# Kernel tuning notes

Hardware: AMD Instinct MI355X
Metric: run time of the kernel (lower is better)

Reference implementation:

```python
import jax, jax.numpy as jnp
import numpy as np

N = 100_000   # nodes
E = 3_200_000 # edges (avg degree 32)
F = 256       # node feature dim
H = 5         # hidden_size (hard-coded in source)
C = 7         # num_classes (hard-coded in source)


def setup_inputs() -> dict:
    key = jax.random.key(0)
    ks = jax.random.split(key, 8)
    x = jax.random.normal(ks[0], (N, F), dtype=jnp.float32)
    edge_index = jax.random.randint(ks[1], (2, E), 0, N, dtype=jnp.int32)
    # GCNConv uses glorot init for weight, zeros for bias; Linear uses kaiming-ish.
    def glorot(k, fan_in, fan_out):
        s = jnp.sqrt(6.0 / (fan_in + fan_out))
        return jax.random.uniform(k, (fan_in, fan_out), jnp.float32, -s, s)
    W1 = glorot(ks[2], F, H)
    b1 = jnp.zeros((H,), jnp.float32)
    W2 = glorot(ks[3], H, H)
    b2 = jnp.zeros((H,), jnp.float32)
    s = 1.0 / jnp.sqrt(jnp.float32(H))
    W3 = jax.random.uniform(ks[4], (H, C), jnp.float32, -s, s)
    b3 = jax.random.uniform(ks[5], (C,), jnp.float32, -s, s)
    return {"x": x, "edge_index": edge_index,
            "W1": W1, "b1": b1, "W2": W2, "b2": b2, "W3": W3, "b3": b3}


def _gcn_conv(h_in, W, b, src, dst, deg_inv_sqrt, n):
    """PyG GCNConv: linear first, then D^-1/2 (A+I) D^-1/2 aggregation, then bias."""
    h = h_in @ W                                   # [N, out]
    norm = deg_inv_sqrt[src] * deg_inv_sqrt[dst]   # [E]
    agg = jax.ops.segment_sum(h[src] * norm[:, None], dst, num_segments=n)
    # self-loop contribution: weight = deg^-1 for each node
    agg = agg + h * (deg_inv_sqrt * deg_inv_sqrt)[:, None]
    return agg + b


def reference(x, edge_index, W1, b1, W2, b2, W3, b3):
    src, dst = edge_index[0], edge_index[1]
    n = x.shape[0]
    # degree with self-loops added (PyG add_self_loops + edge_weight=1)
    deg = jax.ops.segment_sum(jnp.ones_like(src, jnp.float32), dst, num_segments=n) + 1.0
    deg_inv_sqrt = jax.lax.rsqrt(deg)
    h = jax.nn.relu(_gcn_conv(x, W1, b1, src, dst, deg_inv_sqrt, n))
    h = jax.nn.relu(_gcn_conv(h, W2, b2, src, dst, deg_inv_sqrt, n))
    return h @ W3 + b3
```

## Files before the change

### kernel.cpp

```cpp
#include <hip/hip_runtime.h>

#define F_DIM 256
#define H 5
#define C 7
#define PAD 8

#define PART_SH 9
#define PART_NODES 512
#define PCAP 20480
#define TILE 2048
#define NPMAX 256
#define CSR_ROUNDS 20

__global__ __launch_bounds__(256) void k_xw1z(const float* __restrict__ x,
                                              const float* __restrict__ W1,
                                              float* __restrict__ hw1,
                                              int* __restrict__ gcur, int n) {
    if (blockIdx.x == 0 && threadIdx.x < NPMAX) gcur[threadIdx.x] = 0;
    int row = blockIdx.x * 256 + threadIdx.x;
    if (row >= n) return;
    const float4* xp = (const float4*)(x + (size_t)row * F_DIM);
    float acc[H] = {0.f, 0.f, 0.f, 0.f, 0.f};
#pragma unroll 8
    for (int f4 = 0; f4 < F_DIM / 4; ++f4) {
        float4 v = xp[f4];
        const float* wp = W1 + f4 * 4 * H;
#pragma unroll
        for (int c = 0; c < H; ++c)
            acc[c] += v.x * wp[c] + v.y * wp[H + c] + v.z * wp[2 * H + c] + v.w * wp[3 * H + c];
    }
    float* o = hw1 + (size_t)row * PAD;
    *reinterpret_cast<float4*>(o) = make_float4(acc[0], acc[1], acc[2], acc[3]);
    o[4] = acc[4];
}

__global__ __launch_bounds__(256) void k_part(const int* __restrict__ src,
                                              const int* __restrict__ dst,
                                              int* __restrict__ gcur,
                                              unsigned int* __restrict__ parr, int E) {
    __shared__ unsigned int s_out[TILE];
    __shared__ unsigned char s_op[TILE];
    __shared__ int s_wcur[4][NPMAX];
    __shared__ int s_hist[NPMAX];
    __shared__ int s_excl[NPMAX];
    __shared__ int s_gbase[NPMAX];

    const int t = threadIdx.x;
    const int w = t >> 6;
    const int t0 = blockIdx.x * TILE;

    for (int i = t; i < 4 * NPMAX; i += 256) ((int*)s_wcur)[i] = 0;
    __syncthreads();

    unsigned int pair[8];
    int pp[8], rk[8];
#pragma unroll
    for (int k = 0; k < 8; ++k) {
        int e = t0 + k * 256 + t;
        if (e < E) {
            int d = dst[e];
            int s = src[e];
            int p = d >> PART_SH;
            pair[k] = ((unsigned)s << PART_SH) | (unsigned)(d & (PART_NODES - 1));
            pp[k] = p;
            rk[k] = atomicAdd(&s_wcur[w][p], 1);
        } else {
            pp[k] = -1;
        }
    }
    __syncthreads();
    {
        int sum = 0;
#pragma unroll
        for (int ww = 0; ww < 4; ++ww) sum += s_wcur[ww][t];
        s_hist[t] = sum;
    }
    __syncthreads();
    if (t < 64) {
        int base = t * 4;
        int loc[4]; int tot = 0;
#pragma unroll
        for (int k = 0; k < 4; ++k) { loc[k] = tot; tot += s_hist[base + k]; }
        int incl = tot;
#pragma unroll
        for (int off = 1; off < 64; off <<= 1) {
            int u = __shfl_up(incl, off, 64);
            if (t >= off) incl += u;
        }
        int excl = incl - tot;
#pragma unroll
        for (int k = 0; k < 4; ++k) s_excl[base + k] = excl + loc[k];
    }
    __syncthreads();
    {
        int run = s_excl[t];
#pragma unroll
        for (int ww = 0; ww < 4; ++ww) { int c = s_wcur[ww][t]; s_wcur[ww][t] = run; run += c; }
        int cnt = s_hist[t];
        s_gbase[t] = (cnt > 0) ? atomicAdd(&gcur[t], cnt) : 0;
    }
    __syncthreads();
#pragma unroll
    for (int k = 0; k < 8; ++k) {
        if (pp[k] >= 0) {
            int pos = s_wcur[w][pp[k]] + rk[k];
            s_out[pos] = pair[k];
            s_op[pos] = (unsigned char)pp[k];
        }
    }
    __syncthreads();
    const int tilecnt = s_excl[NPMAX - 1] + s_hist[NPMAX - 1];
#pragma unroll
    for (int k = 0; k < 8; ++k) {
        int i = k * 256 + t;
        if (i < tilecnt) {
            int p = s_op[i];
            int gpos = s_gbase[p] + (i - s_excl[p]);
            if (gpos < PCAP)
                parr[(size_t)p * PCAP + gpos] = s_out[i];
        }
    }
}

__global__ __launch_bounds__(1024) void k_csr(
        const int* __restrict__ gcur, const unsigned int* __restrict__ parr,
        int* __restrict__ sorted, int2* __restrict__ rpd, float* __restrict__ dis,
        const float* __restrict__ hw1, float* __restrict__ hw1s, int n) {
    __shared__ int s_cnt[PART_NODES];
    __shared__ int s_excl[PART_NODES];
    const int p = blockIdx.x;
    const int t = threadIdx.x;
    int m = gcur[p]; if (m > PCAP) m = PCAP;
    const unsigned int* pp = parr + (size_t)p * PCAP;

    if (t < PART_NODES) s_cnt[t] = 0;
    __syncthreads();

    unsigned int pr[CSR_ROUNDS];
    int rk[CSR_ROUNDS];
#pragma unroll
    for (int k = 0; k < CSR_ROUNDS; ++k) {
        int i = k * 1024 + t;
        if (i < m) {
            pr[k] = pp[i];
            rk[k] = atomicAdd(&s_cnt[pr[k] & (PART_NODES - 1)], 1);
        }
    }
    __syncthreads();
    if (t < 64) {
        int base = t * 8;
        int loc[8]; int tot = 0;
#pragma unroll
        for (int k = 0; k < 8; ++k) { loc[k] = tot; tot += s_cnt[base + k]; }
        int incl = tot;
#pragma unroll
        for (int off = 1; off < 64; off <<= 1) {
            int u = __shfl_up(incl, off, 64);
            if (t >= off) incl += u;
        }
        int excl = incl - tot;
#pragma unroll
        for (int k = 0; k < 8; ++k) s_excl[base + k] = excl + loc[k];
    }
    __syncthreads();
    if (t < PART_NODES) {
        int node = p * PART_NODES + t;
        if (node < n) {
            int dg = s_cnt[t];
            rpd[node] = make_int2(p * PCAP + s_excl[t], dg);
            float di = rsqrtf((float)dg + 1.0f);
            dis[node] = di;
            const float* hp = hw1 + (size_t)node * PAD;
            float4 a = *(const float4*)hp;
            float h4 = hp[4];
            float* os = hw1s + (size_t)node * PAD;
            *reinterpret_cast<float4*>(os) = make_float4(a.x * di, a.y * di, a.z * di, a.w * di);
            os[4] = h4 * di;
        }
    }
#pragma unroll
    for (int k = 0; k < CSR_ROUNDS; ++k) {
        int i = k * 1024 + t;
        if (i < m) {
            int dloc = pr[k] & (PART_NODES - 1);
            sorted[(size_t)p * PCAP + s_excl[dloc] + rk[k]] = (int)(pr[k] >> PART_SH);
        }
    }
}

template<int OUTD, int OSTRIDE, bool ADD_B3, bool SCALE_OUT>
__global__ __launch_bounds__(256) void k_layer(
        const int* __restrict__ sorted, const int2* __restrict__ rpd,
        const float* __restrict__ dis,
        const float* __restrict__ hin, const float* __restrict__ bn,
        const float* __restrict__ Wnext, const float* __restrict__ b3,
        float* __restrict__ outp, int n) {
    int tid = blockIdx.x * blockDim.x + threadIdx.x;
    int node = tid >> 2, sub = tid & 3;
    if (node >= n) return;
    int2 rd = rpd[node];
    int deg = rd.y;
    const int* bp = sorted + rd.x;

    float acc[H] = {0.f, 0.f, 0.f, 0.f, 0.f};
    int j = sub;
    for (; j + 32 <= deg; j += 32) {
        int s0 = bp[j], s1 = bp[j + 4], s2 = bp[j + 8], s3 = bp[j + 12];
        int s4 = bp[j + 16], s5 = bp[j + 20], s6 = bp[j + 24], s7 = bp[j + 28];
        const float4* h0 = (const float4*)(hin + (size_t)s0 * PAD);
        const float4* h1 = (const float4*)(hin + (size_t)s1 * PAD);
        const float4* h2 = (const float4*)(hin + (size_t)s2 * PAD);
        const float4* h3 = (const float4*)(hin + (size_t)s3 * PAD);
        const float4* h4 = (const float4*)(hin + (size_t)s4 * PAD);
        const float4* h5 = (const float4*)(hin + (size_t)s5 * PAD);
        const float4* h6 = (const float4*)(hin + (size_t)s6 * PAD);
        const float4* h7 = (const float4*)(hin + (size_t)s7 * PAD);
        float4 a0 = h0[0], e0 = h0[1], a1 = h1[0], e1 = h1[1];
        float4 a2 = h2[0], e2 = h2[1], a3 = h3[0], e3 = h3[1];
        float4 a4 = h4[0], e4 = h4[1], a5 = h5[0], e5 = h5[1];
        float4 a6 = h6[0], e6 = h6[1], a7 = h7[0], e7 = h7[1];
        acc[0] += (a0.x + a1.x + a2.x + a3.x) + (a4.x + a5.x + a6.x + a7.x);
        acc[1] += (a0.y + a1.y + a2.y + a3.y) + (a4.y + a5.y + a6.y + a7.y);
        acc[2] += (a0.z + a1.z + a2.z + a3.z) + (a4.z + a5.z + a6.z + a7.z);
        acc[3] += (a0.w + a1.w + a2.w + a3.w) + (a4.w + a5.w + a6.w + a7.w);
        acc[4] += (e0.x + e1.x + e2.x + e3.x) + (e4.x + e5.x + e6.x + e7.x);
    }
    for (; j + 16 <= deg; j += 16) {
        int s0 = bp[j], s1 = bp[j + 4], s2 = bp[j + 8], s3 = bp[j + 12];
        const float4* h0 = (const float4*)(hin + (size_t)s0 * PAD);
        const float4* h1 = (const float4*)(hin + (size_t)s1 * PAD);
        const float4* h2 = (const float4*)(hin + (size_t)s2 * PAD);
        const float4* h3 = (const float4*)(hin + (size_t)s3 * PAD);
        float4 a0 = h0[0], e0 = h0[1], a1 = h1[0], e1 = h1[1];
        float4 a2 = h2[0], e2 = h2[1], a3 = h3[0], e3 = h3[1];
        acc[0] += a0.x + a1.x + a2.x + a3.x;
        acc[1] += a0.y + a1.y + a2.y + a3.y;
        acc[2] += a0.z + a1.z + a2.z + a3.z;
        acc[3] += a0.w + a1.w + a2.w + a3.w;
        acc[4] += e0.x + e1.x + e2.x + e3.x;
    }
    for (; j + 8 <= deg; j += 8) {
        int s0 = bp[j], s1 = bp[j + 4];
        const float4* h0 = (const float4*)(hin + (size_t)s0 * PAD);
        const float4* h1 = (const float4*)(hin + (size_t)s1 * PAD);
        float4 a0 = h0[0], e0 = h0[1], a1 = h1[0], e1 = h1[1];
        acc[0] += a0.x + a1.x;
        acc[1] += a0.y + a1.y;
        acc[2] += a0.z + a1.z;
        acc[3] += a0.w + a1.w;
        acc[4] += e0.x + e1.x;
    }
    for (; j < deg; j += 4) {
        int s0 = bp[j];
        const float4* h0 = (const float4*)(hin + (size_t)s0 * PAD);
        float4 a0 = h0[0], e0 = h0[1];
        acc[0] += a0.x;
        acc[1] += a0.y;
        acc[2] += a0.z;
        acc[3] += a0.w;
        acc[4] += e0.x;
    }
#pragma unroll
    for (int c = 0; c < H; ++c) {
        acc[c] += __shfl_xor(acc[c], 1, 64);
        acc[c] += __shfl_xor(acc[c], 2, 64);
    }
    if (sub != 0) return;

    float di = dis[node];
    const float4* hp4 = (const float4*)(hin + (size_t)node * PAD);
    float4 ha = hp4[0];
    float h4 = hin[(size_t)node * PAD + 4];
    float hself[H] = {ha.x, ha.y, ha.z, ha.w, h4};
    float tt[H];
#pragma unroll
    for (int c = 0; c < H; ++c) {
        float v = (acc[c] + hself[c]) * di + bn[c];
        tt[c] = v > 0.f ? v : 0.f;
    }
    float* op = outp + (size_t)node * OSTRIDE;
#pragma unroll
    for (int c2 = 0; c2 < OUTD; ++c2) {
        float a = ADD_B3 ? b3[c2] : 0.f;
#pragma unroll
        for (int c = 0; c < H; ++c) a += tt[c] * Wnext[c * OUTD + c2];
        op[c2] = SCALE_OUT ? a * di : a;
    }
}

extern "C" void kernel_launch(void* const* d_in, const int* in_sizes, int n_in,
                              void* d_out, int out_size, void* d_ws, size_t ws_size,
                              hipStream_t stream) {
    const float* x  = (const float*)d_in[0];
    const int*   ei = (const int*)d_in[1];
    const float* W1 = (const float*)d_in[2];
    const float* b1 = (const float*)d_in[3];
    const float* W2 = (const float*)d_in[4];
    const float* b2 = (const float*)d_in[5];
    const float* W3 = (const float*)d_in[6];
    const float* b3 = (const float*)d_in[7];
    float* out = (float*)d_out;

    const int n = in_sizes[0] / F_DIM;
    const int E = in_sizes[1] / 2;
    const int* src = ei;
    const int* dst = ei + E;
    const int np = (n + PART_NODES - 1) / PART_NODES;

    char* ws = (char*)d_ws;
    size_t off = 0;
    int* gcur = (int*)(ws + off);                   off += NPMAX * 4;
    unsigned int* parr = (unsigned int*)(ws + off); off += (size_t)np * PCAP * 4;
    int* sorted = (int*)(ws + off);                 off += (size_t)np * PCAP * 4;
    int2* rpd = (int2*)(ws + off);                  off += (size_t)n * 8;
    float* dis = (float*)(ws + off);                off += (size_t)n * 4;
    float* hw1 = (float*)(ws + off);                off += (size_t)n * PAD * 4;
    float* hw1s = (float*)(ws + off);               off += (size_t)n * PAD * 4;
    float* hw2 = (float*)(ws + off);                off += (size_t)n * PAD * 4;

    const int nbp = (E + TILE - 1) / TILE;
    const int nbx = (n + 255) / 256;
    const int nb4 = (4 * n + 255) / 256;

    k_xw1z<<<nbx, 256, 0, stream>>>(x, W1, hw1, gcur, n);
    k_part<<<nbp, 256, 0, stream>>>(src, dst, gcur, parr, E);
    k_csr<<<np, 1024, 0, stream>>>(gcur, parr, sorted, rpd, dis, hw1, hw1s, n);
    k_layer<H, PAD, false, true><<<nb4, 256, 0, stream>>>(
        sorted, rpd, dis, hw1s, b1, W2, nullptr, hw2, n);
    k_layer<C, C, true, false><<<nb4, 256, 0, stream>>>(
        sorted, rpd, dis, hw2, b2, W3, b3, out, n);
}
```

Baseline: 148.7 us.

## Fuse partition with XW1 and replace global bucket atomics with per-tile offsets

The feature projection and the edge-partition pass now run in a single launch, with blocks split by index, so the x·W1 streaming can overlap the partitioning. Partitioning no longer reserves space in global per-partition buckets with atomics. Each tile writes its locally bucketed edges contiguously along with a per-tile exclusive-offset table. The CSR kernel then has each thread walk the matching slice of every tile twice, once to count and once to scatter with shared-memory cursors. This removes the global atomics, the per-partition capacity clamp on the first pass and one kernel launch. In exchange, CSR reads become short serial, poorly coalesced segments spread over many tiles, and the data is read twice.

```diff
diff --git a/kernel.cpp b/kernel.cpp
--- a/kernel.cpp
+++ b/kernel.cpp
@@ -10,141 +10,126 @@
 #define PCAP 20480
 #define TILE 2048
 #define NPMAX 256
-#define CSR_ROUNDS 20
-
-__global__ __launch_bounds__(256) void k_xw1z(const float* __restrict__ x,
-                                              const float* __restrict__ W1,
-                                              float* __restrict__ hw1,
-                                              int* __restrict__ gcur, int n) {
-    if (blockIdx.x == 0 && threadIdx.x < NPMAX) gcur[threadIdx.x] = 0;
-    int row = blockIdx.x * 256 + threadIdx.x;
-    if (row >= n) return;
-    const float4* xp = (const float4*)(x + (size_t)row * F_DIM);
-    float acc[H] = {0.f, 0.f, 0.f, 0.f, 0.f};
+
+__global__ __launch_bounds__(256) void k_pxw(
+        const int* __restrict__ src, const int* __restrict__ dst,
+        unsigned int* __restrict__ parr2, int* __restrict__ excl, int E, int np, int nbp,
+        const float* __restrict__ x, const float* __restrict__ W1,
+        float* __restrict__ hw1, int n) {
+    const int t = threadIdx.x;
+    if ((int)blockIdx.x < nbp) {
+        __shared__ unsigned int s_out[TILE];
+        __shared__ int s_wcur[4][NPMAX];
+        __shared__ int s_hist[NPMAX];
+        __shared__ int s_excl[NPMAX];
+        const int w = t >> 6;
+        const int tile = blockIdx.x;
+        const int t0 = tile * TILE;
+
+        for (int i = t; i < 4 * NPMAX; i += 256) ((int*)s_wcur)[i] = 0;
+        __syncthreads();
+
+        unsigned int pair[8];
+        int pp[8], rk[8];
+#pragma unroll
+        for (int k = 0; k < 8; ++k) {
+            int e = t0 + k * 256 + t;
+            if (e < E) {
+                int d = dst[e];
+                int s = src[e];
+                int p = d >> PART_SH;
+                pair[k] = ((unsigned)s << PART_SH) | (unsigned)(d & (PART_NODES - 1));
+                pp[k] = p;
+                rk[k] = atomicAdd(&s_wcur[w][p], 1);
+            } else {
+                pp[k] = -1;
+            }
+        }
+        __syncthreads();
+        {
+            int sum = 0;
+#pragma unroll
+            for (int ww = 0; ww < 4; ++ww) sum += s_wcur[ww][t];
+            s_hist[t] = sum;
+        }
+        __syncthreads();
+        if (t < 64) {
+            int base = t * 4;
+            int loc[4]; int tot = 0;
+#pragma unroll
+            for (int k = 0; k < 4; ++k) { loc[k] = tot; tot += s_hist[base + k]; }
+            int incl = tot;
+#pragma unroll
+            for (int off = 1; off < 64; off <<= 1) {
+                int u = __shfl_up(incl, off, 64);
+                if (t >= off) incl += u;
+            }
+            int ex = incl - tot;
+#pragma unroll
+            for (int k = 0; k < 4; ++k) s_excl[base + k] = ex + loc[k];
+        }
+        __syncthreads();
+        {
+            int run = s_excl[t];
+#pragma unroll
+            for (int ww = 0; ww < 4; ++ww) { int c = s_wcur[ww][t]; s_wcur[ww][t] = run; run += c; }
+        }
+        __syncthreads();
+#pragma unroll
+        for (int k = 0; k < 8; ++k) {
+            if (pp[k] >= 0) {
+                int pos = s_wcur[w][pp[k]] + rk[k];
+                s_out[pos] = pair[k];
+            }
+        }
+        if (t <= np) excl[(size_t)tile * NPMAX + t] = s_excl[t];
+        __syncthreads();
+        const int tilecnt = s_excl[NPMAX - 1] + s_hist[NPMAX - 1];
+#pragma unroll
+        for (int k = 0; k < 8; ++k) {
+            int i = k * 256 + t;
+            if (i < tilecnt)
+                parr2[(size_t)tile * TILE + i] = s_out[i];
+        }
+    } else {
+        int row = ((int)blockIdx.x - nbp) * 256 + t;
+        if (row >= n) return;
+        const float4* xp = (const float4*)(x + (size_t)row * F_DIM);
+        float acc[H] = {0.f, 0.f, 0.f, 0.f, 0.f};
 #pragma unroll 8
-    for (int f4 = 0; f4 < F_DIM / 4; ++f4) {
-        float4 v = xp[f4];
-        const float* wp = W1 + f4 * 4 * H;
-#pragma unroll
-        for (int c = 0; c < H; ++c)
-            acc[c] += v.x * wp[c] + v.y * wp[H + c] + v.z * wp[2 * H + c] + v.w * wp[3 * H + c];
-    }
-    float* o = hw1 + (size_t)row * PAD;
-    *reinterpret_cast<float4*>(o) = make_float4(acc[0], acc[1], acc[2], acc[3]);
-    o[4] = acc[4];
+        for (int f4 = 0; f4 < F_DIM / 4; ++f4) {
+            float4 v = xp[f4];
+            const float* wp = W1 + f4 * 4 * H;
+#pragma unroll
+            for (int c = 0; c < H; ++c)
+                acc[c] += v.x * wp[c] + v.y * wp[H + c] + v.z * wp[2 * H + c] + v.w * wp[3 * H + c];
+        }
+        float* o = hw1 + (size_t)row * PAD;
+        *reinterpret_cast<float4*>(o) = make_float4(acc[0], acc[1], acc[2], acc[3]);
+        o[4] = acc[4];
+    }
 }
 
-__global__ __launch_bounds__(256) void k_part(const int* __restrict__ src,
-                                              const int* __restrict__ dst,
-                                              int* __restrict__ gcur,
-                                              unsigned int* __restrict__ parr, int E) {
-    __shared__ unsigned int s_out[TILE];
-    __shared__ unsigned char s_op[TILE];
-    __shared__ int s_wcur[4][NPMAX];
-    __shared__ int s_hist[NPMAX];
-    __shared__ int s_excl[NPMAX];
-    __shared__ int s_gbase[NPMAX];
-
-    const int t = threadIdx.x;
-    const int w = t >> 6;
-    const int t0 = blockIdx.x * TILE;
-
-    for (int i = t; i < 4 * NPMAX; i += 256) ((int*)s_wcur)[i] = 0;
-    __syncthreads();
-
-    unsigned int pair[8];
-    int pp[8], rk[8];
-#pragma unroll
-    for (int k = 0; k < 8; ++k) {
-        int e = t0 + k * 256 + t;
-        if (e < E) {
-            int d = dst[e];
-            int s = src[e];
-            int p = d >> PART_SH;
-            pair[k] = ((unsigned)s << PART_SH) | (unsigned)(d & (PART_NODES - 1));
-            pp[k] = p;
-            rk[k] = atomicAdd(&s_wcur[w][p], 1);
-        } else {
-            pp[k] = -1;
-        }
-    }
-    __syncthreads();
-    {
-        int sum = 0;
-#pragma unroll
-        for (int ww = 0; ww < 4; ++ww) sum += s_wcur[ww][t];
-        s_hist[t] = sum;
-    }
-    __syncthreads();
-    if (t < 64) {
-        int base = t * 4;
-        int loc[4]; int tot = 0;
-#pragma unroll
-        for (int k = 0; k < 4; ++k) { loc[k] = tot; tot += s_hist[base + k]; }
-        int incl = tot;
-#pragma unroll
-        for (int off = 1; off < 64; off <<= 1) {
-            int u = __shfl_up(incl, off, 64);
-            if (t >= off) incl += u;
-        }
-        int excl = incl - tot;
-#pragma unroll
-        for (int k = 0; k < 4; ++k) s_excl[base + k] = excl + loc[k];
-    }
-    __syncthreads();
-    {
-        int run = s_excl[t];
-#pragma unroll
-        for (int ww = 0; ww < 4; ++ww) { int c = s_wcur[ww][t]; s_wcur[ww][t] = run; run += c; }
-        int cnt = s_hist[t];
-        s_gbase[t] = (cnt > 0) ? atomicAdd(&gcur[t], cnt) : 0;
-    }
-    __syncthreads();
-#pragma unroll
-    for (int k = 0; k < 8; ++k) {
-        if (pp[k] >= 0) {
-            int pos = s_wcur[w][pp[k]] + rk[k];
-            s_out[pos] = pair[k];
-            s_op[pos] = (unsigned char)pp[k];
-        }
-    }
-    __syncthreads();
-    const int tilecnt = s_excl[NPMAX - 1] + s_hist[NPMAX - 1];
-#pragma unroll
-    for (int k = 0; k < 8; ++k) {
-        int i = k * 256 + t;
-        if (i < tilecnt) {
-            int p = s_op[i];
-            int gpos = s_gbase[p] + (i - s_excl[p]);
-            if (gpos < PCAP)
-                parr[(size_t)p * PCAP + gpos] = s_out[i];
-        }
-    }
-}
-
 __global__ __launch_bounds__(1024) void k_csr(
-        const int* __restrict__ gcur, const unsigned int* __restrict__ parr,
-        int* __restrict__ sorted, int2* __restrict__ rpd, float* __restrict__ dis,
-        const float* __restrict__ hw1, float* __restrict__ hw1s, int n) {
+        const unsigned int* __restrict__ parr2, const int* __restrict__ excl,
+        int ntiles, int* __restrict__ sorted, int2* __restrict__ rpd,
+        float* __restrict__ dis, const float* __restrict__ hw1,
+        float* __restrict__ hw1s, int n) {
     __shared__ int s_cnt[PART_NODES];
-    __shared__ int s_excl[PART_NODES];
+    __shared__ int s_ex[PART_NODES];
+    __shared__ int s_cur[PART_NODES];
     const int p = blockIdx.x;
     const int t = threadIdx.x;
-    int m = gcur[p]; if (m > PCAP) m = PCAP;
-    const unsigned int* pp = parr + (size_t)p * PCAP;
 
     if (t < PART_NODES) s_cnt[t] = 0;
     __syncthreads();
 
-    unsigned int pr[CSR_ROUNDS];
-    int rk[CSR_ROUNDS];
-#pragma unroll
-    for (int k = 0; k < CSR_ROUNDS; ++k) {
-        int i = k * 1024 + t;
-        if (i < m) {
-            pr[k] = pp[i];
-            rk[k] = atomicAdd(&s_cnt[pr[k] & (PART_NODES - 1)], 1);
-        }
+    for (int tile = t; tile < ntiles; tile += 1024) {
+        int e0 = excl[(size_t)tile * NPMAX + p];
+        int e1 = excl[(size_t)tile * NPMAX + p + 1];
+        const unsigned int* base = parr2 + (size_t)tile * TILE;
+        for (int i = e0; i < e1; ++i)
+            atomicAdd(&s_cnt[base[i] & (PART_NODES - 1)], 1);
     }
     __syncthreads();
     if (t < 64) {
@@ -158,16 +143,17 @@
             int u = __shfl_up(incl, off, 64);
             if (t >= off) incl += u;
         }
-        int excl = incl - tot;
-#pragma unroll
-        for (int k = 0; k < 8; ++k) s_excl[base + k] = excl + loc[k];
+        int ex = incl - tot;
+#pragma unroll
+        for (int k = 0; k < 8; ++k) s_ex[base + k] = ex + loc[k];
     }
     __syncthreads();
     if (t < PART_NODES) {
+        s_cur[t] = s_ex[t];
         int node = p * PART_NODES + t;
         if (node < n) {
             int dg = s_cnt[t];
-            rpd[node] = make_int2(p * PCAP + s_excl[t], dg);
+            rpd[node] = make_int2(p * PCAP + s_ex[t], dg);
             float di = rsqrtf((float)dg + 1.0f);
             dis[node] = di;
             const float* hp = hw1 + (size_t)node * PAD;
@@ -178,12 +164,15 @@
             os[4] = h4 * di;
         }
     }
-#pragma unroll
-    for (int k = 0; k < CSR_ROUNDS; ++k) {
-        int i = k * 1024 + t;
-        if (i < m) {
-            int dloc = pr[k] & (PART_NODES - 1);
-            sorted[(size_t)p * PCAP + s_excl[dloc] + rk[k]] = (int)(pr[k] >> PART_SH);
+    __syncthreads();
+    for (int tile = t; tile < ntiles; tile += 1024) {
+        int e0 = excl[(size_t)tile * NPMAX + p];
+        int e1 = excl[(size_t)tile * NPMAX + p + 1];
+        const unsigned int* base = parr2 + (size_t)tile * TILE;
+        for (int i = e0; i < e1; ++i) {
+            unsigned int pr = base[i];
+            int pos = atomicAdd(&s_cur[pr & (PART_NODES - 1)], 1);
+            sorted[(size_t)p * PCAP + pos] = (int)(pr >> PART_SH);
         }
     }
 }
@@ -306,25 +295,24 @@
     const int* src = ei;
     const int* dst = ei + E;
     const int np = (n + PART_NODES - 1) / PART_NODES;
+    const int nbp = (E + TILE - 1) / TILE;
+    const int nbx = (n + 255) / 256;
 
     char* ws = (char*)d_ws;
     size_t off = 0;
-    int* gcur = (int*)(ws + off);                   off += NPMAX * 4;
-    unsigned int* parr = (unsigned int*)(ws + off); off += (size_t)np * PCAP * 4;
-    int* sorted = (int*)(ws + off);                 off += (size_t)np * PCAP * 4;
-    int2* rpd = (int2*)(ws + off);                  off += (size_t)n * 8;
-    float* dis = (float*)(ws + off);                off += (size_t)n * 4;
-    float* hw1 = (float*)(ws + off);                off += (size_t)n * PAD * 4;
-    float* hw1s = (float*)(ws + off);               off += (size_t)n * PAD * 4;
-    float* hw2 = (float*)(ws + off);                off += (size_t)n * PAD * 4;
-
-    const int nbp = (E + TILE - 1) / TILE;
-    const int nbx = (n + 255) / 256;
+    unsigned int* parr2 = (unsigned int*)(ws + off); off += (size_t)nbp * TILE * 4;
+    int* excl = (int*)(ws + off);                    off += (size_t)nbp * NPMAX * 4;
+    int* sorted = (int*)(ws + off);                  off += (size_t)np * PCAP * 4;
+    int2* rpd = (int2*)(ws + off);                   off += (size_t)n * 8;
+    float* dis = (float*)(ws + off);                 off += (size_t)n * 4;
+    float* hw1 = (float*)(ws + off);                 off += (size_t)n * PAD * 4;
+    float* hw1s = (float*)(ws + off);                off += (size_t)n * PAD * 4;
+    float* hw2 = (float*)(ws + off);                 off += (size_t)n * PAD * 4;
+
     const int nb4 = (4 * n + 255) / 256;
 
-    k_xw1z<<<nbx, 256, 0, stream>>>(x, W1, hw1, gcur, n);
-    k_part<<<nbp, 256, 0, stream>>>(src, dst, gcur, parr, E);
-    k_csr<<<np, 1024, 0, stream>>>(gcur, parr, sorted, rpd, dis, hw1, hw1s, n);
+    k_pxw<<<nbp + nbx, 256, 0, stream>>>(src, dst, parr2, excl, E, np, nbp, x, W1, hw1, n);
+    k_csr<<<np, 1024, 0, stream>>>(parr2, excl, nbp, sorted, rpd, dis, hw1, hw1s, n);
     k_layer<H, PAD, false, true><<<nb4, 256, 0, stream>>>(
         sorted, rpd, dis, hw1s, b1, W2, nullptr, hw2, n);
     k_layer<C, C, true, false><<<nb4, 256, 0, stream>>>(
```

Result: slower. 170.7 us (+14.8%).
